# Optimization experiments

Measured on AMD Instinct MI355X. Metric: run time of the kernel, lower is better.

The kernel has to match this reference:

```python
import jax, jax.numpy as jnp
import numpy as np

N_PTS = 262144
N_FREQ_COOR = 10
N_FREQ_DIR = 4
D = 8
W = 256
INPUT_CH = 3 + 3 * N_FREQ_COOR * 2        # 63
INPUT_CH_DIR = 3 + 3 * N_FREQ_DIR * 2     # 27
SKIPS = (4,)
SIGMA_MUL = 0.0


def embed(x, n_freqs):
    freqs = (2.0 ** jnp.arange(n_freqs)).astype(x.dtype)      # [F]
    xf = x[..., None, :] * freqs[:, None]                      # [N, F, 3]
    sc = jnp.stack([jnp.sin(xf), jnp.cos(xf)], axis=-2)        # [N, F, 2, 3]
    sc = sc.reshape(*x.shape[:-1], n_freqs * 2 * x.shape[-1])  # [N, F*2*3]
    return jnp.concatenate([x, sc], axis=-1)


def _linear_params(key, fan_in, fan_out):
    kw, kb = jax.random.split(key)
    s = 1.0 / np.sqrt(fan_in)
    Wm = jax.random.uniform(kw, (fan_out, fan_in), jnp.float32, -s, s)
    b = jax.random.uniform(kb, (fan_out,), jnp.float32, -s, s)
    return Wm, b


def setup_inputs() -> dict:
    key = jax.random.key(0)
    keys = jax.random.split(key, 16)
    inp = {}
    inp['pts'] = jax.random.normal(keys[0], (N_PTS, 3), jnp.float32)
    inp['dirs'] = jax.random.normal(keys[1], (N_PTS, 3), jnp.float32)
    inp['dirs'] = inp['dirs'] / jnp.linalg.norm(inp['dirs'], axis=-1, keepdims=True)
    # base layer dims (skip concat before layer 5)
    dims_in = [INPUT_CH, W, W, W, W, W + INPUT_CH, W, W]
    for i in range(D):
        Wm, b = _linear_params(keys[2 + i], dims_in[i], W)
        inp[f'Wb{i}'] = Wm
        inp[f'bb{i}'] = b
    inp['Wsig'], inp['bsig'] = _linear_params(keys[10], W, 1)
    inp['Wrm'], inp['brm'] = _linear_params(keys[11], W, 256)
    inp['Wr0'], inp['br0'] = _linear_params(keys[12], 256 + INPUT_CH_DIR, W // 2)
    inp['Wr1'], inp['br1'] = _linear_params(keys[13], W // 2, 3)
    return inp


def _forward(pts, dirs,
             Wb0, bb0, Wb1, bb1, Wb2, bb2, Wb3, bb3,
             Wb4, bb4, Wb5, bb5, Wb6, bb6, Wb7, bb7,
             Wsig, bsig, Wrm, brm, Wr0, br0, Wr1, br1):
    p = embed(pts, N_FREQ_COOR)   # [N, 63]
    d = embed(dirs, N_FREQ_DIR)   # [N, 27]
    Ws = [Wb0, Wb1, Wb2, Wb3, Wb4, Wb5, Wb6, Wb7]
    bs = [bb0, bb1, bb2, bb3, bb4, bb5, bb6, bb7]
    base = jax.nn.relu(p @ Ws[0].T + bs[0])
    for i in range(D - 1):
        if i in SKIPS:
            base = jnp.concatenate([p, base], axis=-1)
        base = jax.nn.relu(base @ Ws[i + 1].T + bs[i + 1])
    sigma = base @ Wsig.T + bsig                     # [N, 1]
    sigma = sigma + jax.nn.relu(sigma) * SIGMA_MUL
    base_remap = jax.nn.relu(base @ Wrm.T + brm)     # [N, 256]
    rgb_fea = jax.nn.relu(jnp.concatenate([base_remap, d], axis=-1) @ Wr0.T + br0)
    rgb = jax.nn.sigmoid(rgb_fea @ Wr1.T + br1)      # [N, 3]
    return rgb, sigma[..., 0], d


def reference(pts, dirs,
              Wb0, bb0, Wb1, bb1, Wb2, bb2, Wb3, bb3,
              Wb4, bb4, Wb5, bb5, Wb6, bb6, Wb7, bb7,
              Wsig, bsig, Wrm, brm, Wr0, br0, Wr1, br1):
    # Returns (rgb, sigma, embedded dirs) matching StyleNerf.execute's OrderedDict values.
    return _forward(pts, dirs,
                    Wb0, bb0, Wb1, bb1, Wb2, bb2, Wb3, bb3,
                    Wb4, bb4, Wb5, bb5, Wb6, bb6, Wb7, bb7,
                    Wsig, bsig, Wrm, brm, Wr0, br0, Wr1, br1)
```

## Files before the change

### kernel.cpp

```cpp
#include <hip/hip_runtime.h>
#include <hip/hip_bf16.h>
#include <math.h>

#define NPTS 262144
#define TM   64
#define NTHR 256
#define AS   272
#define PS   80

#define WS_SHORTS 593920

typedef short  short8  __attribute__((ext_vector_type(8)));
typedef float  floatx4 __attribute__((ext_vector_type(4)));

__device__ __forceinline__ unsigned short f2b(float f) {
  union { float f; unsigned int i; } v; v.f = f;
  return (unsigned short)((v.i + 0x7fffu + ((v.i >> 16) & 1u)) >> 16);
}
__device__ __forceinline__ float b2f(unsigned short u) {
  union { unsigned int i; float f; } v; v.i = ((unsigned int)u) << 16; return v.f;
}

struct PrepArgs {
  const float* src[10];
  unsigned short* ws;
  long long dst[10];
  int steps[10];
  int ksrc[10];
  int mode[10];
  int nf16[10];
};

__global__ __launch_bounds__(256) void prep_weights(PrepArgs P) {
  int jl = blockIdx.x, c = blockIdx.y;
  if (c >= P.steps[jl]) return;
  const int NF = P.nf16[jl], tot = NF * 512;
  const float* src = P.src[jl];
  const int Ks = P.ksrc[jl], mode = P.mode[jl];
  unsigned short* dst = P.ws + P.dst[jl] + (long long)c * tot;
  for (int u = threadIdx.x; u < tot; u += 256) {
    int j = u & 7, lane = (u >> 3) & 63, nf = u >> 9;
    int n  = nf * 16 + (lane & 15);
    int kp = c * 32 + ((lane >> 4) << 3) + j;
    int sc;
    if (mode == 0)      sc = kp;
    else if (mode == 1) sc = (kp < Ks) ? kp : -1;
    else                sc = (kp < 256) ? kp + 63 : (kp < Ks ? kp - 256 : -1);
    dst[u] = (sc >= 0) ? f2b(src[(long long)n * Ks + sc]) : (unsigned short)0;
  }
}

struct NerfArgs {
  const float* pts;
  const float* dirs;
  const unsigned short* ws;
  const float* bias[10];
  const float* Wsig;
  const float* bsig;
  const float* Wr1;
  const float* br1;
  float* out;
};

template<int NFTOT, int NFW, int STEPS, int STEPS0, int LD0, int LD1>
__device__ __forceinline__ void gemm_g(
    const unsigned short* wimg,
    const short* seg0, const short* seg1,
    const float* bias, short* dst, int tid)
{
  const int lane = tid & 63, wave = tid >> 6;
  const int prow = lane & 15;
  const int r4   = (lane >> 4) * 4;
  const int koff = (lane >> 4) * 8;

  floatx4 acc[4][NFW];
  {
    float4 bv[NFW];
#pragma unroll
    for (int i = 0; i < NFW; ++i)
      bv[i] = *(const float4*)(bias + (wave * NFW + i) * 16 + r4);
#pragma unroll
    for (int mf = 0; mf < 4; ++mf)
#pragma unroll
      for (int i = 0; i < NFW; ++i) {
        acc[mf][i][0] = bv[i].x; acc[mf][i][1] = bv[i].y;
        acc[mf][i][2] = bv[i].z; acc[mf][i][3] = bv[i].w;
      }
  }

  const unsigned short* wl = wimg + (size_t)(wave * NFW) * 512 + (size_t)lane * 8;
  const short* b0 = seg0 + (size_t)prow * LD0 + koff;
  const short* b1 = seg1 + (size_t)prow * LD1 + koff;

  short8 wreg[3][NFW];
#pragma unroll
  for (int i = 0; i < NFW; ++i) wreg[0][i] = *(const short8*)(wl + i * 512);
  if (STEPS > 1) {
#pragma unroll
    for (int i = 0; i < NFW; ++i)
      wreg[1][i] = *(const short8*)(wl + (size_t)(NFTOT * 512) + i * 512);
  }

#pragma unroll
  for (int s = 0; s < STEPS; ++s) {
    if (s + 2 < STEPS) {
      const unsigned short* wn = wl + (size_t)(s + 2) * (NFTOT * 512);
#pragma unroll
      for (int i = 0; i < NFW; ++i)
        wreg[(s + 2) % 3][i] = *(const short8*)(wn + i * 512);
    }
    short8 b[4];
#pragma unroll
    for (int mf = 0; mf < 4; ++mf) {
      if (s < STEPS0) b[mf] = *(const short8*)(b0 + mf * 16 * LD0 + s * 32);
      else            b[mf] = *(const short8*)(b1 + mf * 16 * LD1 + (s - STEPS0) * 32);
    }
    __builtin_amdgcn_s_setprio(1);
#pragma unroll
    for (int mf = 0; mf < 4; ++mf)
#pragma unroll
      for (int i = 0; i < NFW; ++i)
        acc[mf][i] = __builtin_amdgcn_mfma_f32_16x16x32_bf16(wreg[s % 3][i], b[mf], acc[mf][i], 0, 0, 0);
    __builtin_amdgcn_s_setprio(0);
  }
  __syncthreads();
  short* dstb = dst + (size_t)prow * AS + wave * NFW * 16 + r4;
#pragma unroll
  for (int i = 0; i < NFW; ++i) {
#pragma unroll
    for (int mf = 0; mf < 4; ++mf) {
      float v0 = fmaxf(acc[mf][i][0], 0.f);
      float v1 = fmaxf(acc[mf][i][1], 0.f);
      float v2 = fmaxf(acc[mf][i][2], 0.f);
      float v3 = fmaxf(acc[mf][i][3], 0.f);
      __hip_bfloat162 h01 = __float22bfloat162_rn(make_float2(v0, v1));
      __hip_bfloat162 h23 = __float22bfloat162_rn(make_float2(v2, v3));
      int2 pk;
      pk.x = *(const int*)&h01;
      pk.y = *(const int*)&h23;
      *(int2*)(dstb + mf * 16 * AS + i * 16) = pk;
    }
  }
  __syncthreads();
}

__global__ __launch_bounds__(NTHR, 3)
void nerf_fused(NerfArgs A) {
  __shared__ alignas(16) short act[TM * AS];
  __shared__ alignas(16) short pbuf[TM * PS];
  const int tid = threadIdx.x;
  const int lane = tid & 63, wave = tid >> 6;
  const size_t gbase = (size_t)blockIdx.x * TM;

  if (tid < 192) {
    int row = tid & 63, dim = tid >> 6;
    float x = A.pts[(gbase + row) * 3 + dim];
    short* pr = pbuf + row * PS;
    pr[dim] = (short)f2b(x);
    float s = 0.f, c = 0.f, fr = 1.f;
#pragma unroll
    for (int q = 0; q < 10; ++q) {
      if ((q & 3) == 0) { s = sinf(x * fr); c = cosf(x * fr); }
      pr[3 + q * 6 + dim]     = (short)f2b(s);
      pr[3 + q * 6 + 3 + dim] = (short)f2b(c);
      float ns = 2.f * s * c;
      float nc = 1.f - 2.f * s * s;
      s = ns; c = nc;
      fr *= 2.f;
    }
  } else {
    pbuf[(tid - 192) * PS + 63] = 0;
  }
  __syncthreads();

  const short* actp = act;
  short*       actw = act;
  const short* pbp  = pbuf;
  const unsigned short* ws = A.ws;

  gemm_g<16, 4,  2, 2, PS, AS>(ws + 0,      pbp,  actp, A.bias[0], actw, tid);
  gemm_g<16, 4,  8, 8, AS, AS>(ws + 16384,  actp, actp, A.bias[1], actw, tid);
  gemm_g<16, 4,  8, 8, AS, AS>(ws + 81920,  actp, actp, A.bias[2], actw, tid);
  gemm_g<16, 4,  8, 8, AS, AS>(ws + 147456, actp, actp, A.bias[3], actw, tid);
  gemm_g<16, 4,  8, 8, AS, AS>(ws + 212992, actp, actp, A.bias[4], actw, tid);
  gemm_g<16, 4, 10, 8, AS, PS>(ws + 278528, actp, pbp,  A.bias[5], actw, tid);

  if (tid >= 64 && tid < 128) {
    int row = tid - 64;
    size_t g = gbase + row;
    float x0 = A.dirs[g * 3 + 0];
    float x1 = A.dirs[g * 3 + 1];
    float x2 = A.dirs[g * 3 + 2];
    float vals[27];
    vals[0] = x0; vals[1] = x1; vals[2] = x2;
    float sx = sinf(x0), cx = cosf(x0);
    float sy = sinf(x1), cy = cosf(x1);
    float sz = sinf(x2), cz = cosf(x2);
#pragma unroll
    for (int q = 0; q < 4; ++q) {
      vals[3 + q * 6 + 0] = sx;
      vals[3 + q * 6 + 1] = sy;
      vals[3 + q * 6 + 2] = sz;
      vals[3 + q * 6 + 3] = cx;
      vals[3 + q * 6 + 4] = cy;
      vals[3 + q * 6 + 5] = cz;
      float nsx = 2.f * sx * cx, ncx = 1.f - 2.f * sx * sx;
      float nsy = 2.f * sy * cy, ncy = 1.f - 2.f * sy * sy;
      float nsz = 2.f * sz * cz, ncz = 1.f - 2.f * sz * sz;
      sx = nsx; cx = ncx; sy = nsy; cy = ncy; sz = nsz; cz = ncz;
    }
    short* dr = pbuf + row * PS;
    float* og = A.out + (size_t)4 * NPTS + g * 27;
    for (int j = 0; j < 27; ++j) {
      dr[j] = (short)f2b(vals[j]);
      og[j] = vals[j];
    }
    for (int j = 27; j < 32; ++j) dr[j] = 0;
  }

  gemm_g<16, 4,  8, 8, AS, AS>(ws + 360448, actp, actp, A.bias[6], actw, tid);
  gemm_g<16, 4,  8, 8, AS, AS>(ws + 425984, actp, actp, A.bias[7], actw, tid);

  {
    int p = wave * 16 + (lane & 15);
    int q = lane >> 4;
    float s = 0.f;
    for (int c8 = 0; c8 < 8; ++c8) {
      int k0 = q * 64 + c8 * 8;
      short8 v = *(const short8*)(act + p * AS + k0);
      const float4 w0 = *(const float4*)(A.Wsig + k0);
      const float4 w1 = *(const float4*)(A.Wsig + k0 + 4);
      s += b2f((unsigned short)v[0]) * w0.x + b2f((unsigned short)v[1]) * w0.y
         + b2f((unsigned short)v[2]) * w0.z + b2f((unsigned short)v[3]) * w0.w
         + b2f((unsigned short)v[4]) * w1.x + b2f((unsigned short)v[5]) * w1.y
         + b2f((unsigned short)v[6]) * w1.z + b2f((unsigned short)v[7]) * w1.w;
    }
    s += __shfl_xor(s, 16);
    s += __shfl_xor(s, 32);
    if (q == 0) A.out[(size_t)3 * NPTS + gbase + p] = s + A.bsig[0];
  }

  gemm_g<16, 4,  8, 8, AS, AS>(ws + 491520, actp, actp, A.bias[8], actw, tid);
  gemm_g< 8, 2,  9, 8, AS, PS>(ws + 557056, actp, pbp,  A.bias[9], actw, tid);

  {
    int p = wave * 16 + (lane & 15);
    int q = lane >> 4;
    float s0 = 0.f, s1 = 0.f, s2 = 0.f;
    for (int c8 = 0; c8 < 4; ++c8) {
      int k0 = q * 32 + c8 * 8;
      short8 v = *(const short8*)(act + p * AS + k0);
#pragma unroll
      for (int j = 0; j < 8; ++j) {
        float fv = b2f((unsigned short)v[j]);
        s0 += fv * A.Wr1[k0 + j];
        s1 += fv * A.Wr1[128 + k0 + j];
        s2 += fv * A.Wr1[256 + k0 + j];
      }
    }
    s0 += __shfl_xor(s0, 16); s0 += __shfl_xor(s0, 32);
    s1 += __shfl_xor(s1, 16); s1 += __shfl_xor(s1, 32);
    s2 += __shfl_xor(s2, 16); s2 += __shfl_xor(s2, 32);
    if (q == 0) {
      size_t g = gbase + p;
      A.out[g * 3 + 0] = 1.f / (1.f + expf(-(s0 + A.br1[0])));
      A.out[g * 3 + 1] = 1.f / (1.f + expf(-(s1 + A.br1[1])));
      A.out[g * 3 + 2] = 1.f / (1.f + expf(-(s2 + A.br1[2])));
    }
  }
}

extern "C" void kernel_launch(void* const* d_in, const int* in_sizes, int n_in,
                              void* d_out, int out_size, void* d_ws, size_t ws_size,
                              hipStream_t stream) {
  PrepArgs pp;
  const int       widx[10]  = {2, 4, 6, 8, 10, 12, 14, 16, 20, 22};
  const long long doffs[10] = {0, 16384, 81920, 147456, 212992, 278528,
                               360448, 425984, 491520, 557056};
  const int stv[10] = {2, 8, 8, 8, 8, 10, 8, 8, 8, 9};
  const int ksv[10] = {63, 256, 256, 256, 256, 319, 256, 256, 256, 283};
  const int mdv[10] = {1, 0, 0, 0, 0, 2, 0, 0, 0, 1};
  const int nfv[10] = {16, 16, 16, 16, 16, 16, 16, 16, 16, 8};
  pp.ws = (unsigned short*)d_ws;
  for (int j = 0; j < 10; ++j) {
    pp.src[j] = (const float*)d_in[widx[j]];
    pp.dst[j] = doffs[j]; pp.steps[j] = stv[j]; pp.ksrc[j] = ksv[j];
    pp.mode[j] = mdv[j]; pp.nf16[j] = nfv[j];
  }
  prep_weights<<<dim3(10, 10), dim3(256), 0, stream>>>(pp);

  NerfArgs na;
  na.pts  = (const float*)d_in[0];
  na.dirs = (const float*)d_in[1];
  na.ws   = (const unsigned short*)d_ws;
  for (int i = 0; i < 8; ++i) na.bias[i] = (const float*)d_in[3 + 2 * i];
  na.bias[8] = (const float*)d_in[21];
  na.bias[9] = (const float*)d_in[23];
  na.Wsig = (const float*)d_in[18];
  na.bsig = (const float*)d_in[19];
  na.Wr1  = (const float*)d_in[24];
  na.br1  = (const float*)d_in[25];
  na.out  = (float*)d_out;
  nerf_fused<<<dim3(NPTS / TM), dim3(NTHR), 0, stream>>>(na);
}
```

Measured before the change: 398.9 us.

## Prefetch next layer's first weight fragments and bias during current GEMM epilogue

Moves the initial weight-register and bias loads for each layer into the tail of the previous layer's GEMM, so the global-memory latency of the next layer's first K-steps overlaps the barrier and activation write-back. The first layer's weights are preloaded before positional encoding. Two explicit __syncthreads are added around the dir-embedding and sigma sections to keep the shared buffers safe. This adds register pressure from the weight and bias arrays that persist across layers, which may affect occupancy at launch bounds of 3 blocks.

```diff
diff --git a/kernel.cpp b/kernel.cpp
--- a/kernel.cpp
+++ b/kernel.cpp
@@ -62,11 +62,14 @@
   float* out;
 };
 
-template<int NFTOT, int NFW, int STEPS, int STEPS0, int LD0, int LD1>
+template<int NFTOT, int NFW, int STEPS, int STEPS0, int LD0, int LD1,
+         int NFT_N, int NFW_N>
 __device__ __forceinline__ void gemm_g(
     const unsigned short* wimg,
     const short* seg0, const short* seg1,
-    const float* bias, short* dst, int tid)
+    short* dst, int tid,
+    short8 wreg[3][4], float4 bv[4],
+    const unsigned short* wnext, const float* bnext)
 {
   const int lane = tid & 63, wave = tid >> 6;
   const int prow = lane & 15;
@@ -74,32 +77,17 @@
   const int koff = (lane >> 4) * 8;
 
   floatx4 acc[4][NFW];
-  {
-    float4 bv[NFW];
-#pragma unroll
-    for (int i = 0; i < NFW; ++i)
-      bv[i] = *(const float4*)(bias + (wave * NFW + i) * 16 + r4);
-#pragma unroll
-    for (int mf = 0; mf < 4; ++mf)
-#pragma unroll
-      for (int i = 0; i < NFW; ++i) {
-        acc[mf][i][0] = bv[i].x; acc[mf][i][1] = bv[i].y;
-        acc[mf][i][2] = bv[i].z; acc[mf][i][3] = bv[i].w;
-      }
-  }
-
-  const unsigned short* wl = wimg + (size_t)(wave * NFW) * 512 + (size_t)lane * 8;
+#pragma unroll
+  for (int mf = 0; mf < 4; ++mf)
+#pragma unroll
+    for (int i = 0; i < NFW; ++i) {
+      acc[mf][i][0] = bv[i].x; acc[mf][i][1] = bv[i].y;
+      acc[mf][i][2] = bv[i].z; acc[mf][i][3] = bv[i].w;
+    }
+
   const short* b0 = seg0 + (size_t)prow * LD0 + koff;
   const short* b1 = seg1 + (size_t)prow * LD1 + koff;
-
-  short8 wreg[3][NFW];
-#pragma unroll
-  for (int i = 0; i < NFW; ++i) wreg[0][i] = *(const short8*)(wl + i * 512);
-  if (STEPS > 1) {
-#pragma unroll
-    for (int i = 0; i < NFW; ++i)
-      wreg[1][i] = *(const short8*)(wl + (size_t)(NFTOT * 512) + i * 512);
-  }
+  const unsigned short* wl = wimg + (size_t)(wave * NFW) * 512 + (size_t)lane * 8;
 
 #pragma unroll
   for (int s = 0; s < STEPS; ++s) {
@@ -123,6 +111,20 @@
         acc[mf][i] = __builtin_amdgcn_mfma_f32_16x16x32_bf16(wreg[s % 3][i], b[mf], acc[mf][i], 0, 0, 0);
     __builtin_amdgcn_s_setprio(0);
   }
+
+  if (NFW_N > 0) {
+    const unsigned short* wn0 = wnext + (size_t)(wave * NFW_N) * 512 + (size_t)lane * 8;
+#pragma unroll
+    for (int i = 0; i < NFW_N; ++i)
+      wreg[0][i] = *(const short8*)(wn0 + i * 512);
+#pragma unroll
+    for (int i = 0; i < NFW_N; ++i)
+      wreg[1][i] = *(const short8*)(wn0 + (size_t)(NFT_N * 512) + i * 512);
+#pragma unroll
+    for (int i = 0; i < NFW_N; ++i)
+      bv[i] = *(const float4*)(bnext + (wave * NFW_N + i) * 16 + r4);
+  }
+
   __syncthreads();
   short* dstb = dst + (size_t)prow * AS + wave * NFW * 16 + r4;
 #pragma unroll
@@ -152,6 +154,19 @@
   const int lane = tid & 63, wave = tid >> 6;
   const size_t gbase = (size_t)blockIdx.x * TM;
 
+  short8 wreg[3][4];
+  float4 bv[4];
+  {
+    const unsigned short* w0 = A.ws + (size_t)(wave * 4) * 512 + (size_t)lane * 8;
+    const int r4 = (lane >> 4) * 4;
+#pragma unroll
+    for (int i = 0; i < 4; ++i) wreg[0][i] = *(const short8*)(w0 + i * 512);
+#pragma unroll
+    for (int i = 0; i < 4; ++i) wreg[1][i] = *(const short8*)(w0 + 16 * 512 + i * 512);
+#pragma unroll
+    for (int i = 0; i < 4; ++i) bv[i] = *(const float4*)(A.bias[0] + (wave * 4 + i) * 16 + r4);
+  }
+
   if (tid < 192) {
     int row = tid & 63, dim = tid >> 6;
     float x = A.pts[(gbase + row) * 3 + dim];
@@ -178,12 +193,12 @@
   const short* pbp  = pbuf;
   const unsigned short* ws = A.ws;
 
-  gemm_g<16, 4,  2, 2, PS, AS>(ws + 0,      pbp,  actp, A.bias[0], actw, tid);
-  gemm_g<16, 4,  8, 8, AS, AS>(ws + 16384,  actp, actp, A.bias[1], actw, tid);
-  gemm_g<16, 4,  8, 8, AS, AS>(ws + 81920,  actp, actp, A.bias[2], actw, tid);
-  gemm_g<16, 4,  8, 8, AS, AS>(ws + 147456, actp, actp, A.bias[3], actw, tid);
-  gemm_g<16, 4,  8, 8, AS, AS>(ws + 212992, actp, actp, A.bias[4], actw, tid);
-  gemm_g<16, 4, 10, 8, AS, PS>(ws + 278528, actp, pbp,  A.bias[5], actw, tid);
+  gemm_g<16, 4,  2, 2, PS, AS, 16, 4>(ws + 0,      pbp,  actp, actw, tid, wreg, bv, ws + 16384,  A.bias[1]);
+  gemm_g<16, 4,  8, 8, AS, AS, 16, 4>(ws + 16384,  actp, actp, actw, tid, wreg, bv, ws + 81920,  A.bias[2]);
+  gemm_g<16, 4,  8, 8, AS, AS, 16, 4>(ws + 81920,  actp, actp, actw, tid, wreg, bv, ws + 147456, A.bias[3]);
+  gemm_g<16, 4,  8, 8, AS, AS, 16, 4>(ws + 147456, actp, actp, actw, tid, wreg, bv, ws + 212992, A.bias[4]);
+  gemm_g<16, 4,  8, 8, AS, AS, 16, 4>(ws + 212992, actp, actp, actw, tid, wreg, bv, ws + 278528, A.bias[5]);
+  gemm_g<16, 4, 10, 8, AS, PS, 16, 4>(ws + 278528, actp, pbp,  actw, tid, wreg, bv, ws + 360448, A.bias[6]);
 
   if (tid >= 64 && tid < 128) {
     int row = tid - 64;
@@ -217,9 +232,10 @@
     }
     for (int j = 27; j < 32; ++j) dr[j] = 0;
   }
-
-  gemm_g<16, 4,  8, 8, AS, AS>(ws + 360448, actp, actp, A.bias[6], actw, tid);
-  gemm_g<16, 4,  8, 8, AS, AS>(ws + 425984, actp, actp, A.bias[7], actw, tid);
+  __syncthreads();
+
+  gemm_g<16, 4,  8, 8, AS, AS, 16, 4>(ws + 360448, actp, actp, actw, tid, wreg, bv, ws + 425984, A.bias[7]);
+  gemm_g<16, 4,  8, 8, AS, AS, 16, 4>(ws + 425984, actp, actp, actw, tid, wreg, bv, ws + 491520, A.bias[8]);
 
   {
     int p = wave * 16 + (lane & 15);
@@ -239,9 +255,10 @@
     s += __shfl_xor(s, 32);
     if (q == 0) A.out[(size_t)3 * NPTS + gbase + p] = s + A.bsig[0];
   }
-
-  gemm_g<16, 4,  8, 8, AS, AS>(ws + 491520, actp, actp, A.bias[8], actw, tid);
-  gemm_g< 8, 2,  9, 8, AS, PS>(ws + 557056, actp, pbp,  A.bias[9], actw, tid);
+  __syncthreads();
+
+  gemm_g<16, 4,  8, 8, AS, AS,  8, 2>(ws + 491520, actp, actp, actw, tid, wreg, bv, ws + 557056, A.bias[9]);
+  gemm_g< 8, 2,  9, 8, AS, PS,  0, 0>(ws + 557056, actp, pbp,  actw, tid, wreg, bv, (const unsigned short*)0, (const float*)0);
 
   {
     int p = wave * 16 + (lane & 15);
```

New measurement: 394.0 us, median of 2. Within noise of the previous version (-1.2%).
